# Kernel optimization log

Hardware: AMD Instinct MI355X
Metric: run time of the kernel (lower is better)

## Reference

```python
import jax, jax.numpy as jnp
import numpy as np

N_NODES = 20000
N_EDGES = 200000
N_GRAPHS = 500
F = 512      # num_features
H = 512      # hidden_dim
C = 10       # num_classes
K = 30       # sort-pool k


def setup_inputs() -> dict:
    key = jax.random.key(0)
    ks = jax.random.split(key, 12)
    p = lambda k, shp: (jax.random.normal(k, shp, jnp.float32) * 0.05)
    x = jax.random.normal(ks[0], (N_NODES, F), jnp.float32)
    edge_index = jax.random.randint(ks[1], (2, N_EDGES), 0, N_NODES, dtype=jnp.int32)
    batch = jnp.sort(jax.random.randint(ks[2], (N_NODES,), 0, N_GRAPHS, dtype=jnp.int32))
    return dict(
        x=x, edge_index=edge_index, batch=batch,
        W1=p(ks[3], (F, H)), b1=jnp.zeros((H,), jnp.float32),
        W2=p(ks[4], (H, H)), b2=jnp.zeros((H,), jnp.float32),
        W3=p(ks[5], (H, 1)), b3=jnp.zeros((1,), jnp.float32),
        cw1=p(ks[6], (16, 1, 2 * H + 1)), cb1=jnp.zeros((16,), jnp.float32),
        cw2=p(ks[7], (32, 16, 5)), cb2=jnp.zeros((32,), jnp.float32),
        lw1=p(ks[8], (352, H)), lb1=jnp.zeros((H,), jnp.float32),
        lw2=p(ks[9], (H, C)), lb2=jnp.zeros((C,), jnp.float32),
    )


def gcn_conv(x, W, b, src, dst):
    # PyG GCNConv: add self-loops, symmetric deg^-1/2 normalization, then scatter-add.
    n = x.shape[0]
    loop = jnp.arange(n, dtype=src.dtype)
    s = jnp.concatenate([src, loop])
    d = jnp.concatenate([dst, loop])
    deg = jax.ops.segment_sum(jnp.ones_like(d, dtype=x.dtype), d, num_segments=n)
    dinv = jnp.where(deg > 0, jax.lax.rsqrt(deg), 0.0)
    norm = dinv[s] * dinv[d]                       # [E+N]
    h = x @ W                                      # transform first (in < out ok)
    out = jax.ops.segment_sum(h[s] * norm[:, None], d, num_segments=n)
    return out + b


def global_sort_pool(feat, batch, num_graphs, k):
    # Sort nodes within each graph by last feature channel (descending),
    # keep first k per graph, zero-pad short graphs. Returns [G, k*D].
    n, D = feat.shape
    key = feat[:, -1]
    order = jnp.lexsort((-key, batch))             # primary: batch asc, secondary: key desc
    bs = batch[order]
    fs = feat[order]
    counts = jax.ops.segment_sum(jnp.ones_like(batch, dtype=jnp.int32), batch, num_segments=num_graphs)
    starts = jnp.cumsum(counts) - counts
    rank = jnp.arange(n, dtype=jnp.int32) - starts[bs]
    valid = rank < k
    pooled = jnp.zeros((num_graphs, k, D), feat.dtype).at[
        bs, jnp.clip(rank, 0, k - 1)
    ].add(jnp.where(valid[:, None], fs, 0.0))
    return pooled.reshape(num_graphs, k * D)


def reference(x, edge_index, batch, W1, b1, W2, b2, W3, b3,
              cw1, cb1, cw2, cb2, lw1, lb1, lw2, lb2):
    src, dst = edge_index[0], edge_index[1]
    x1 = jax.nn.elu(gcn_conv(x, W1, b1, src, dst))                 # dropout = identity (eval)
    x2 = jax.nn.elu(gcn_conv(x1, W2, b2, src, dst) + x1)
    out = gcn_conv(x2, W3, b3, src, dst)                           # [N, 1]
    feat = jnp.concatenate([x1, x2, out], axis=-1)                 # [N, 2H+1]
    D = feat.shape[-1]
    z = global_sort_pool(feat, batch, N_GRAPHS, K)                 # [G, K*D]
    z = z[:, None, :]                                              # [G, 1, K*D]
    dn = ('NCH', 'OIH', 'NCH')
    z = jax.nn.relu(jax.lax.conv_general_dilated(z, cw1, (D,), 'VALID', dimension_numbers=dn) + cb1[None, :, None])  # [G,16,30]
    z = jax.lax.reduce_window(z, -jnp.inf, jax.lax.max, (1, 1, 2), (1, 1, 2), 'VALID')                               # [G,16,15]
    z = jax.nn.relu(jax.lax.conv_general_dilated(z, cw2, (1,), 'VALID', dimension_numbers=dn) + cb2[None, :, None])  # [G,32,11]
    z = z.reshape(z.shape[0], -1)                                  # [G,352]
    z = jax.nn.relu(z @ lw1 + lb1)
    return z @ lw2 + lb2                                           # [G, C]
```

## Files before the change

### kernel.cpp

```cpp
#include <hip/hip_runtime.h>
#include <hip/hip_bf16.h>

#define NN 20000
#define NEDGE 200000
#define NG 500
#define KTOP 30
#define HDIM 512

typedef __attribute__((ext_vector_type(8))) short s16x8;
typedef __attribute__((ext_vector_type(4))) float f32x4;

__device__ __forceinline__ unsigned short f2bf(float f) {
    unsigned int u = __float_as_uint(f);
    return (unsigned short)((u + 0x7FFFu + ((u >> 16) & 1u)) >> 16);
}
__device__ __forceinline__ float bf2f(unsigned short s) {
    return __uint_as_float(((unsigned int)s) << 16);
}


__global__ void k_init(int* indeg, int* ccur, int* gcnt) {
    int i = blockIdx.x * 256 + threadIdx.x;
    if (i < NN) { indeg[i] = 0; ccur[i] = 0; }
    if (i < NG) gcnt[i] = 0;
}

__global__ void k_count(const int* __restrict__ dst, int* indeg, int ne) {
    int e = blockIdx.x * 256 + threadIdx.x;
    if (e < ne) atomicAdd(&indeg[dst[e]], 1);
}

__global__ void k_gcount(const int* __restrict__ batch, int* gcnt) {
    int i = blockIdx.x * 256 + threadIdx.x;
    if (i < NN) atomicAdd(&gcnt[batch[i]], 1);
}

__global__ void k_dinv(const int* __restrict__ indeg, float* dinv) {
    int i = blockIdx.x * 256 + threadIdx.x;
    if (i < NN) dinv[i] = rsqrtf((float)(indeg[i] + 1));
}

__global__ void k_scan(const int* __restrict__ in, int* __restrict__ out, int n) {
    const int NT = 256;
    __shared__ int sums[NT];
    int t = threadIdx.x;
    int per = (n + NT - 1) / NT;
    int s0 = t * per;
    int local = 0;
    for (int k = 0; k < per; ++k) { int idx = s0 + k; if (idx < n) local += in[idx]; }
    sums[t] = local;
    __syncthreads();
    for (int off = 1; off < NT; off <<= 1) {
        int v = (t >= off) ? sums[t - off] : 0;
        __syncthreads();
        sums[t] += v;
        __syncthreads();
    }
    int run = sums[t] - local;
    for (int k = 0; k < per; ++k) { int idx = s0 + k; if (idx < n) { out[idx] = run; run += in[idx]; } }
    if (t == NT - 1) out[n] = run;
}

__global__ void k_fill(const int* __restrict__ src, const int* __restrict__ dst,
                       const int* __restrict__ cstart, int* ccur, int* csrc, int ne) {
    int e = blockIdx.x * 256 + threadIdx.x;
    if (e < ne) {
        int d = dst[e];
        int pos = cstart[d] + atomicAdd(&ccur[d], 1);
        csrc[pos] = src[e];
    }
}


__global__ __launch_bounds__(256) void k_split(const float* __restrict__ A,
                                               unsigned short* __restrict__ o0,
                                               unsigned short* __restrict__ o1,
                                               unsigned short* __restrict__ o2, int n4) {
    int i = blockIdx.x * 256 + threadIdx.x;
    if (i >= n4) return;
    float4 v = ((const float4*)A)[i];
    float f[4] = {v.x, v.y, v.z, v.w};
    unsigned short h0[4], h1[4], h2[4];
    #pragma unroll
    for (int j = 0; j < 4; ++j) {
        h0[j] = f2bf(f[j]);   float r = f[j] - bf2f(h0[j]);
        h1[j] = f2bf(r);      r -= bf2f(h1[j]);
        h2[j] = f2bf(r);
    }
    ((ushort4*)o0)[i] = make_ushort4(h0[0], h0[1], h0[2], h0[3]);
    ((ushort4*)o1)[i] = make_ushort4(h1[0], h1[1], h1[2], h1[3]);
    ((ushort4*)o2)[i] = make_ushort4(h2[0], h2[1], h2[2], h2[3]);
}

__global__ __launch_bounds__(256) void k_splitW(const float* __restrict__ W,
                                                unsigned short* __restrict__ w0,
                                                unsigned short* __restrict__ w1,
                                                unsigned short* __restrict__ w2) {
    __shared__ float tile[32][33];
    int bk = blockIdx.x * 32, bn = blockIdx.y * 32;
    int tx = threadIdx.x & 31, ty = threadIdx.x >> 5;
    #pragma unroll
    for (int r = 0; r < 4; ++r)
        tile[ty * 4 + r][tx] = W[(size_t)(bk + ty * 4 + r) * 512 + bn + tx];
    __syncthreads();
    #pragma unroll
    for (int r = 0; r < 4; ++r) {
        int n = bn + ty * 4 + r, k = bk + tx;
        float v = tile[tx][ty * 4 + r];
        unsigned short a0 = f2bf(v); float rr = v - bf2f(a0);
        unsigned short a1 = f2bf(rr); rr -= bf2f(a1);
        w0[(size_t)n * 512 + k] = a0;
        w1[(size_t)n * 512 + k] = a1;
        w2[(size_t)n * 512 + k] = f2bf(rr);
    }
}


#define ASTR (NN * HDIM)
#define BSTR (512 * 512)

__global__ __launch_bounds__(256) void k_gemm_mfma(const unsigned short* __restrict__ S,
                                                   const unsigned short* __restrict__ Wt,
                                                   float* __restrict__ C, int M) {
    __shared__ short lds[6][4096];
    const int t = threadIdx.x;
    const int lane = t & 63, wid = t >> 6;
    const int wr = wid >> 1, wc = wid & 1;
    const int bm = blockIdx.x * 128, bn = blockIdx.y * 128;
    const int arow = lane & 15, koff = (lane >> 4) * 8;

    int offA[6], offB[6], ldsA[6], ldsB[6];
    #pragma unroll
    for (int i = 0; i < 6; ++i) {
        int u = i * 4 + wid;
        int c = u >> 3, g = u & 7;
        int row = bm + g * 16 + arow; if (row >= M) row = M - 1;
        offA[i] = c * ASTR + row * HDIM + koff;
        ldsA[i] = c * 4096 + (g * 64 + lane) * 8;
    }
    #pragma unroll
    for (int i = 0; i < 6; ++i) {
        int u = i * 4 + wid;
        int c = u >> 3, g = u & 7;
        int row = bn + g * 16 + arow;
        offB[i] = c * BSTR + row * 512 + koff;
        ldsB[i] = (3 + c) * 4096 + (g * 64 + lane) * 8;
    }

    f32x4 acc[4][4];
    #pragma unroll
    for (int m = 0; m < 4; ++m)
        #pragma unroll
        for (int n = 0; n < 4; ++n) acc[m][n] = (f32x4){0.f, 0.f, 0.f, 0.f};

    s16x8 stA[6], stB[6];
    #pragma unroll
    for (int i = 0; i < 6; ++i) stA[i] = *(const s16x8*)(S + offA[i]);
    #pragma unroll
    for (int i = 0; i < 6; ++i) stB[i] = *(const s16x8*)(Wt + offB[i]);

    short* lp = &lds[0][0];
    #pragma unroll 1
    for (int s = 0; s < 16; ++s) {
        __syncthreads();
        #pragma unroll
        for (int i = 0; i < 6; ++i) *(s16x8*)(lp + ldsA[i]) = stA[i];
        #pragma unroll
        for (int i = 0; i < 6; ++i) *(s16x8*)(lp + ldsB[i]) = stB[i];
        if (s + 1 < 16) {
            int kadv = (s + 1) * 32;
            #pragma unroll
            for (int i = 0; i < 6; ++i) stA[i] = *(const s16x8*)(S + offA[i] + kadv);
            #pragma unroll
            for (int i = 0; i < 6; ++i) stB[i] = *(const s16x8*)(Wt + offB[i] + kadv);
        }
        __syncthreads();
        s16x8 af[3][4], bf[3][4];
        #pragma unroll
        for (int c = 0; c < 3; ++c)
            #pragma unroll
            for (int m = 0; m < 4; ++m)
                af[c][m] = *(const s16x8*)(lp + c * 4096 + ((wr * 4 + m) * 64 + lane) * 8);
        #pragma unroll
        for (int c = 0; c < 3; ++c)
            #pragma unroll
            for (int n = 0; n < 4; ++n)
                bf[c][n] = *(const s16x8*)(lp + (3 + c) * 4096 + ((wc * 4 + n) * 64 + lane) * 8);
        #pragma unroll
        for (int m = 0; m < 4; ++m)
            #pragma unroll
            for (int n = 0; n < 4; ++n) {
                acc[m][n] = __builtin_amdgcn_mfma_f32_16x16x32_bf16(af[0][m], bf[0][n], acc[m][n], 0, 0, 0);
                acc[m][n] = __builtin_amdgcn_mfma_f32_16x16x32_bf16(af[0][m], bf[1][n], acc[m][n], 0, 0, 0);
                acc[m][n] = __builtin_amdgcn_mfma_f32_16x16x32_bf16(af[1][m], bf[0][n], acc[m][n], 0, 0, 0);
                acc[m][n] = __builtin_amdgcn_mfma_f32_16x16x32_bf16(af[0][m], bf[2][n], acc[m][n], 0, 0, 0);
                acc[m][n] = __builtin_amdgcn_mfma_f32_16x16x32_bf16(af[1][m], bf[1][n], acc[m][n], 0, 0, 0);
                acc[m][n] = __builtin_amdgcn_mfma_f32_16x16x32_bf16(af[2][m], bf[0][n], acc[m][n], 0, 0, 0);
            }
    }

    int crow0 = bm + wr * 64 + (lane >> 4) * 4;
    int ccol0 = bn + wc * 64 + (lane & 15);
    #pragma unroll
    for (int m = 0; m < 4; ++m)
        #pragma unroll
        for (int n = 0; n < 4; ++n)
            #pragma unroll
            for (int r = 0; r < 4; ++r) {
                int row = crow0 + m * 16 + r;
                if (row < M) C[(size_t)row * 512 + ccol0 + n * 16] = acc[m][n][r];
            }
}


__global__ __launch_bounds__(256) void k_agg(const float* __restrict__ h, const int* __restrict__ cstart,
                                             const int* __restrict__ csrc, const float* __restrict__ dinv,
                                             const float* __restrict__ bias, const float* __restrict__ res,
                                             float* __restrict__ out) {
    int w = blockIdx.x * 4 + (threadIdx.x >> 6);
    if (w >= NN) return;
    int lane = threadIdx.x & 63;
    float di = dinv[w];
    float acc[8] = {0, 0, 0, 0, 0, 0, 0, 0};
    int e0 = cstart[w], e1 = cstart[w + 1];
    for (int j = e0; j < e1; ++j) {
        int s = csrc[j];
        float wt = dinv[s] * di;
        const float* hr = h + (size_t)s * HDIM + lane * 8;
        float4 v0 = *(const float4*)hr;
        float4 v1 = *(const float4*)(hr + 4);
        acc[0] = fmaf(v0.x, wt, acc[0]); acc[1] = fmaf(v0.y, wt, acc[1]);
        acc[2] = fmaf(v0.z, wt, acc[2]); acc[3] = fmaf(v0.w, wt, acc[3]);
        acc[4] = fmaf(v1.x, wt, acc[4]); acc[5] = fmaf(v1.y, wt, acc[5]);
        acc[6] = fmaf(v1.z, wt, acc[6]); acc[7] = fmaf(v1.w, wt, acc[7]);
    }
    {
        float wt = di * di;
        const float* hr = h + (size_t)w * HDIM + lane * 8;
        float4 v0 = *(const float4*)hr;
        float4 v1 = *(const float4*)(hr + 4);
        acc[0] = fmaf(v0.x, wt, acc[0]); acc[1] = fmaf(v0.y, wt, acc[1]);
        acc[2] = fmaf(v0.z, wt, acc[2]); acc[3] = fmaf(v0.w, wt, acc[3]);
        acc[4] = fmaf(v1.x, wt, acc[4]); acc[5] = fmaf(v1.y, wt, acc[5]);
        acc[6] = fmaf(v1.z, wt, acc[6]); acc[7] = fmaf(v1.w, wt, acc[7]);
    }
    const float* bptr = bias + lane * 8;
    const float* rptr = res ? res + (size_t)w * HDIM + lane * 8 : nullptr;
    float v[8];
    #pragma unroll
    for (int q = 0; q < 8; ++q) {
        float t = acc[q] + bptr[q];
        if (rptr) t += rptr[q];
        v[q] = t > 0.f ? t : (expf(t) - 1.f);
    }
    float* orow = out + (size_t)w * HDIM + lane * 8;
    *(float4*)orow       = make_float4(v[0], v[1], v[2], v[3]);
    *(float4*)(orow + 4) = make_float4(v[4], v[5], v[6], v[7]);
}


__global__ __launch_bounds__(256) void k_gemv3(const float* __restrict__ x2, const float* __restrict__ W3,
                                               float* __restrict__ h3) {
    int w = blockIdx.x * 4 + (threadIdx.x >> 6);
    if (w >= NN) return;
    int lane = threadIdx.x & 63;
    const float* r = x2 + (size_t)w * HDIM + lane * 8;
    const float* wp = W3 + lane * 8;
    float4 a0 = *(const float4*)r, a1 = *(const float4*)(r + 4);
    float4 w0 = *(const float4*)wp, w1 = *(const float4*)(wp + 4);
    float acc = a0.x * w0.x + a0.y * w0.y + a0.z * w0.z + a0.w * w0.w
              + a1.x * w1.x + a1.y * w1.y + a1.z * w1.z + a1.w * w1.w;
    #pragma unroll
    for (int off = 32; off; off >>= 1) acc += __shfl_down(acc, off);
    if (lane == 0) h3[w] = acc;
}

__global__ void k_agg3(const float* __restrict__ h3, const int* __restrict__ cstart,
                       const int* __restrict__ csrc, const float* __restrict__ dinv,
                       const float* __restrict__ b3, float* __restrict__ key) {
    int i = blockIdx.x * 256 + threadIdx.x;
    if (i >= NN) return;
    float di = dinv[i];
    float acc = h3[i] * di * di;
    int e0 = cstart[i], e1 = cstart[i + 1];
    for (int j = e0; j < e1; ++j) {
        int s = csrc[j];
        acc = fmaf(h3[s], dinv[s] * di, acc);
    }
    key[i] = acc + b3[0];
}


#define MAXN 2048
__global__ __launch_bounds__(256) void k_select(const float* __restrict__ key, const int* __restrict__ gstart,
                                                int* __restrict__ sel) {
    int g = blockIdx.x;
    int s = gstart[g], e = gstart[g + 1];
    int cnt = e - s;
    if (cnt > MAXN) cnt = MAXN;
    __shared__ float ks[MAXN];
    __shared__ int sels[KTOP];
    for (int i = threadIdx.x; i < cnt; i += 256) ks[i] = key[s + i];
    if (threadIdx.x < KTOP) sels[threadIdx.x] = -1;
    __syncthreads();
    for (int i = threadIdx.x; i < cnt; i += 256) {
        float ki = ks[i];
        int r = 0;
        for (int j = 0; j < cnt; ++j) {
            float kj = ks[j];
            r += (kj > ki) || (kj == ki && j < i);
        }
        if (r < KTOP) sels[r] = s + i;
    }
    __syncthreads();
    if (threadIdx.x < KTOP) sel[g * KTOP + threadIdx.x] = sels[threadIdx.x];
}


__global__ __launch_bounds__(256) void k_conv1(const float* __restrict__ x1, const float* __restrict__ x2,
                                               const float* __restrict__ key, const int* __restrict__ sel,
                                               const float* __restrict__ cw1, const float* __restrict__ cb1,
                                               float* __restrict__ c1) {
    int gp = blockIdx.x;
    int g = gp / KTOP, p = gp - g * KTOP;
    int t = threadIdx.x;
    int node = sel[gp];
    if (node < 0) {
        if (t < 16) c1[((size_t)g * 16 + t) * KTOP + p] = fmaxf(cb1[t], 0.f);
        return;
    }
    __shared__ float f[1025];
    __shared__ float red[16][17];
    if (t < 128) {
        ((float4*)f)[t] = ((const float4*)(x1 + (size_t)node * HDIM))[t];
    } else {
        ((float4*)(f + 512))[t - 128] = ((const float4*)(x2 + (size_t)node * HDIM))[t - 128];
    }
    if (t == 0) f[1024] = key[node];
    __syncthreads();
    int oc = t >> 4, ch = t & 15;
    const float* wrow = cw1 + (size_t)oc * 1025;
    float pd = 0.f;
    for (int k = ch; k < 1025; k += 16) pd = fmaf(f[k], wrow[k], pd);
    red[oc][ch] = pd;
    __syncthreads();
    if (t < 16) {
        float ssum = cb1[t];
        #pragma unroll
        for (int c = 0; c < 16; ++c) ssum += red[t][c];
        c1[((size_t)g * 16 + t) * KTOP + p] = fmaxf(ssum, 0.f);
    }
}


__global__ __launch_bounds__(512) void k_head(const float* __restrict__ c1, const float* __restrict__ cw2,
                                              const float* __restrict__ cb2, const float* __restrict__ lw1,
                                              const float* __restrict__ lb1, const float* __restrict__ lw2,
                                              const float* __restrict__ lb2, float* __restrict__ outp) {
    int g = blockIdx.x, t = threadIdx.x;
    __shared__ float m[16][15];
    __shared__ float z2s[352];
    __shared__ float z3[512];
    if (t < 240) {
        int ic = t / 15, q = t % 15;
        const float* row = c1 + ((size_t)g * 16 + ic) * KTOP;
        m[ic][q] = fmaxf(row[2 * q], row[2 * q + 1]);
    }
    __syncthreads();
    if (t < 352) {
        int oc = t / 11, tt = t % 11;
        float acc = cb2[oc];
        #pragma unroll
        for (int ic = 0; ic < 16; ++ic)
            #pragma unroll
            for (int j = 0; j < 5; ++j)
                acc = fmaf(m[ic][tt + j], cw2[((size_t)oc * 16 + ic) * 5 + j], acc);
        z2s[t] = fmaxf(acc, 0.f);
    }
    __syncthreads();
    {
        float acc = lb1[t];
        for (int k = 0; k < 352; ++k) acc = fmaf(z2s[k], lw1[(size_t)k * 512 + t], acc);
        z3[t] = fmaxf(acc, 0.f);
    }
    __syncthreads();
    if (t < 160) {
        int oc = t >> 4, l = t & 15;
        float acc = 0.f;
        for (int k = l; k < 512; k += 16) acc = fmaf(z3[k], lw2[(size_t)k * 10 + oc], acc);
        #pragma unroll
        for (int off = 1; off < 16; off <<= 1) acc += __shfl_xor(acc, off);
        if (l == 0) outp[g * 10 + oc] = acc + lb2[oc];
    }
}


extern "C" void kernel_launch(void* const* d_in, const int* in_sizes, int n_in,
                              void* d_out, int out_size, void* d_ws, size_t ws_size,
                              hipStream_t stream) {
    const float* x    = (const float*)d_in[0];
    const int*   ei   = (const int*)d_in[1];
    const int*   batch= (const int*)d_in[2];
    const float* W1   = (const float*)d_in[3];
    const float* b1   = (const float*)d_in[4];
    const float* W2   = (const float*)d_in[5];
    const float* b2   = (const float*)d_in[6];
    const float* W3   = (const float*)d_in[7];
    const float* b3   = (const float*)d_in[8];
    const float* cw1  = (const float*)d_in[9];
    const float* cb1  = (const float*)d_in[10];
    const float* cw2  = (const float*)d_in[11];
    const float* cb2  = (const float*)d_in[12];
    const float* lw1  = (const float*)d_in[13];
    const float* lb1  = (const float*)d_in[14];
    const float* lw2  = (const float*)d_in[15];
    const float* lb2  = (const float*)d_in[16];

    const int NE = in_sizes[1] / 2;
    const int* srcp = ei;
    const int* dstp = ei + NE;

    char* ws = (char*)d_ws;
    size_t o = 0;
    auto al = [&](size_t b) { size_t r = o; o += (b + 255) & ~(size_t)255; return r; };
    int*   indeg  = (int*)(ws + al((size_t)NN * 4));
    int*   ccur   = (int*)(ws + al((size_t)NN * 4));
    int*   cstart = (int*)(ws + al((size_t)(NN + 1) * 4));
    int*   csrc   = (int*)(ws + al((size_t)NE * 4));
    float* dinv   = (float*)(ws + al((size_t)NN * 4));
    float* h      = (float*)(ws + al((size_t)NN * HDIM * 4));
    float* x1     = (float*)(ws + al((size_t)NN * HDIM * 4));
    float* h3     = (float*)(ws + al((size_t)NN * 4));
    float* key    = (float*)(ws + al((size_t)NN * 4));
    int*   gcnt   = (int*)(ws + al((size_t)NG * 4));
    int*   gstart = (int*)(ws + al((size_t)(NG + 1) * 4));
    int*   sel    = (int*)(ws + al((size_t)NG * KTOP * 4));
    float* c1     = (float*)(ws + al((size_t)NG * 16 * KTOP * 4));
    unsigned short* S  = (unsigned short*)(ws + al((size_t)3 * NN * HDIM * 2));
    unsigned short* Wt = (unsigned short*)(ws + al((size_t)3 * 512 * 512 * 2));
    float* x2 = (float*)S;
    (void)ws_size; (void)n_in; (void)out_size;

    int nb_n = (NN + 255) / 256;
    int nb_e = (NE + 255) / 256;

    k_init<<<nb_n, 256, 0, stream>>>(indeg, ccur, gcnt);
    k_count<<<nb_e, 256, 0, stream>>>(dstp, indeg, NE);
    k_gcount<<<nb_n, 256, 0, stream>>>(batch, gcnt);
    k_dinv<<<nb_n, 256, 0, stream>>>(indeg, dinv);
    k_scan<<<1, 256, 0, stream>>>(indeg, cstart, NN);
    k_scan<<<1, 256, 0, stream>>>(gcnt, gstart, NG);
    k_fill<<<nb_e, 256, 0, stream>>>(srcp, dstp, cstart, ccur, csrc, NE);

    const int n4 = NN * HDIM / 4;
    const int nsp = (n4 + 255) / 256;
    dim3 gw(16, 16);
    dim3 gg((NN + 127) / 128, 4);

    k_split<<<nsp, 256, 0, stream>>>(x, S, S + (size_t)NN * HDIM, S + (size_t)2 * NN * HDIM, n4);
    k_splitW<<<gw, 256, 0, stream>>>(W1, Wt, Wt + 512 * 512, Wt + 2 * 512 * 512);
    k_gemm_mfma<<<gg, 256, 0, stream>>>(S, Wt, h, NN);
    k_agg<<<NN / 4, 256, 0, stream>>>(h, cstart, csrc, dinv, b1, nullptr, x1);
    k_split<<<nsp, 256, 0, stream>>>(x1, S, S + (size_t)NN * HDIM, S + (size_t)2 * NN * HDIM, n4);
    k_splitW<<<gw, 256, 0, stream>>>(W2, Wt, Wt + 512 * 512, Wt + 2 * 512 * 512);
    k_gemm_mfma<<<gg, 256, 0, stream>>>(S, Wt, h, NN);
    k_agg<<<NN / 4, 256, 0, stream>>>(h, cstart, csrc, dinv, b2, x1, x2);
    k_gemv3<<<NN / 4, 256, 0, stream>>>(x2, W3, h3);
    k_agg3<<<nb_n, 256, 0, stream>>>(h3, cstart, csrc, dinv, b3, key);
    k_select<<<NG, 256, 0, stream>>>(key, gstart, sel);
    k_conv1<<<NG * KTOP, 256, 0, stream>>>(x1, x2, key, sel, cw1, cb1, c1);
    k_head<<<NG, 512, 0, stream>>>(c1, cw2, cb2, lw1, lb1, lw2, lb2, (float*)d_out);
}
```

Baseline: 684.0 us.

## Fuse bf16 split into aggregation, halve GEMM M-tile, unroll edge loop by two

The first aggregation kernel now writes the three-way bf16 split of its output directly, which removes a separate k_split pass that re-read x1 from memory. The MFMA GEMM tile shrinks from 128 to 64 rows, doubling the block count to improve occupancy and load balance across CUs, at the cost of more B-tile reloads. The aggregation edge loop is unrolled by two with separate accumulators to keep more gather loads in flight. The extra accumulators slightly change summation order and raise register use.

```diff
diff --git a/kernel.cpp b/kernel.cpp
--- a/kernel.cpp
+++ b/kernel.cpp
@@ -122,21 +122,21 @@
 __global__ __launch_bounds__(256) void k_gemm_mfma(const unsigned short* __restrict__ S,
                                                    const unsigned short* __restrict__ Wt,
                                                    float* __restrict__ C, int M) {
-    __shared__ short lds[6][4096];
+    __shared__ short lds[18432];
     const int t = threadIdx.x;
     const int lane = t & 63, wid = t >> 6;
     const int wr = wid >> 1, wc = wid & 1;
-    const int bm = blockIdx.x * 128, bn = blockIdx.y * 128;
+    const int bm = blockIdx.x * 64, bn = blockIdx.y * 128;
     const int arow = lane & 15, koff = (lane >> 4) * 8;
 
-    int offA[6], offB[6], ldsA[6], ldsB[6];
-    #pragma unroll
-    for (int i = 0; i < 6; ++i) {
+    int offA[3], offB[6], ldsA[3], ldsB[6];
+    #pragma unroll
+    for (int i = 0; i < 3; ++i) {
         int u = i * 4 + wid;
-        int c = u >> 3, g = u & 7;
+        int c = u >> 2, g = u & 3;
         int row = bm + g * 16 + arow; if (row >= M) row = M - 1;
         offA[i] = c * ASTR + row * HDIM + koff;
-        ldsA[i] = c * 4096 + (g * 64 + lane) * 8;
+        ldsA[i] = c * 2048 + (g * 64 + lane) * 8;
     }
     #pragma unroll
     for (int i = 0; i < 6; ++i) {
@@ -144,50 +144,50 @@
         int c = u >> 3, g = u & 7;
         int row = bn + g * 16 + arow;
         offB[i] = c * BSTR + row * 512 + koff;
-        ldsB[i] = (3 + c) * 4096 + (g * 64 + lane) * 8;
-    }
-
-    f32x4 acc[4][4];
-    #pragma unroll
-    for (int m = 0; m < 4; ++m)
+        ldsB[i] = 6144 + c * 4096 + (g * 64 + lane) * 8;
+    }
+
+    f32x4 acc[2][4];
+    #pragma unroll
+    for (int m = 0; m < 2; ++m)
         #pragma unroll
         for (int n = 0; n < 4; ++n) acc[m][n] = (f32x4){0.f, 0.f, 0.f, 0.f};
 
-    s16x8 stA[6], stB[6];
-    #pragma unroll
-    for (int i = 0; i < 6; ++i) stA[i] = *(const s16x8*)(S + offA[i]);
+    s16x8 stA[3], stB[6];
+    #pragma unroll
+    for (int i = 0; i < 3; ++i) stA[i] = *(const s16x8*)(S + offA[i]);
     #pragma unroll
     for (int i = 0; i < 6; ++i) stB[i] = *(const s16x8*)(Wt + offB[i]);
 
-    short* lp = &lds[0][0];
+    short* lp = lds;
     #pragma unroll 1
     for (int s = 0; s < 16; ++s) {
         __syncthreads();
         #pragma unroll
-        for (int i = 0; i < 6; ++i) *(s16x8*)(lp + ldsA[i]) = stA[i];
+        for (int i = 0; i < 3; ++i) *(s16x8*)(lp + ldsA[i]) = stA[i];
         #pragma unroll
         for (int i = 0; i < 6; ++i) *(s16x8*)(lp + ldsB[i]) = stB[i];
         if (s + 1 < 16) {
             int kadv = (s + 1) * 32;
             #pragma unroll
-            for (int i = 0; i < 6; ++i) stA[i] = *(const s16x8*)(S + offA[i] + kadv);
+            for (int i = 0; i < 3; ++i) stA[i] = *(const s16x8*)(S + offA[i] + kadv);
             #pragma unroll
             for (int i = 0; i < 6; ++i) stB[i] = *(const s16x8*)(Wt + offB[i] + kadv);
         }
         __syncthreads();
-        s16x8 af[3][4], bf[3][4];
+        s16x8 af[3][2], bf[3][4];
         #pragma unroll
         for (int c = 0; c < 3; ++c)
             #pragma unroll
-            for (int m = 0; m < 4; ++m)
-                af[c][m] = *(const s16x8*)(lp + c * 4096 + ((wr * 4 + m) * 64 + lane) * 8);
+            for (int m = 0; m < 2; ++m)
+                af[c][m] = *(const s16x8*)(lp + c * 2048 + ((wr * 2 + m) * 64 + lane) * 8);
         #pragma unroll
         for (int c = 0; c < 3; ++c)
             #pragma unroll
             for (int n = 0; n < 4; ++n)
-                bf[c][n] = *(const s16x8*)(lp + (3 + c) * 4096 + ((wc * 4 + n) * 64 + lane) * 8);
-        #pragma unroll
-        for (int m = 0; m < 4; ++m)
+                bf[c][n] = *(const s16x8*)(lp + 6144 + c * 4096 + ((wc * 4 + n) * 64 + lane) * 8);
+        #pragma unroll
+        for (int m = 0; m < 2; ++m)
             #pragma unroll
             for (int n = 0; n < 4; ++n) {
                 acc[m][n] = __builtin_amdgcn_mfma_f32_16x16x32_bf16(af[0][m], bf[0][n], acc[m][n], 0, 0, 0);
@@ -199,10 +199,10 @@
             }
     }
 
-    int crow0 = bm + wr * 64 + (lane >> 4) * 4;
+    int crow0 = bm + wr * 32 + (lane >> 4) * 4;
     int ccol0 = bn + wc * 64 + (lane & 15);
     #pragma unroll
-    for (int m = 0; m < 4; ++m)
+    for (int m = 0; m < 2; ++m)
         #pragma unroll
         for (int n = 0; n < 4; ++n)
             #pragma unroll
@@ -216,14 +216,35 @@
 __global__ __launch_bounds__(256) void k_agg(const float* __restrict__ h, const int* __restrict__ cstart,
                                              const int* __restrict__ csrc, const float* __restrict__ dinv,
                                              const float* __restrict__ bias, const float* __restrict__ res,
-                                             float* __restrict__ out) {
+                                             float* __restrict__ out,
+                                             unsigned short* __restrict__ o0,
+                                             unsigned short* __restrict__ o1,
+                                             unsigned short* __restrict__ o2) {
     int w = blockIdx.x * 4 + (threadIdx.x >> 6);
     if (w >= NN) return;
     int lane = threadIdx.x & 63;
     float di = dinv[w];
     float acc[8] = {0, 0, 0, 0, 0, 0, 0, 0};
+    float acc2[8] = {0, 0, 0, 0, 0, 0, 0, 0};
     int e0 = cstart[w], e1 = cstart[w + 1];
-    for (int j = e0; j < e1; ++j) {
+    int j = e0;
+    for (; j + 1 < e1; j += 2) {
+        int s0 = csrc[j], s1 = csrc[j + 1];
+        float wt0 = dinv[s0] * di, wt1 = dinv[s1] * di;
+        const float* hr0 = h + (size_t)s0 * HDIM + lane * 8;
+        const float* hr1 = h + (size_t)s1 * HDIM + lane * 8;
+        float4 a0 = *(const float4*)hr0, a1 = *(const float4*)(hr0 + 4);
+        float4 b0 = *(const float4*)hr1, b1 = *(const float4*)(hr1 + 4);
+        acc[0] = fmaf(a0.x, wt0, acc[0]); acc[1] = fmaf(a0.y, wt0, acc[1]);
+        acc[2] = fmaf(a0.z, wt0, acc[2]); acc[3] = fmaf(a0.w, wt0, acc[3]);
+        acc[4] = fmaf(a1.x, wt0, acc[4]); acc[5] = fmaf(a1.y, wt0, acc[5]);
+        acc[6] = fmaf(a1.z, wt0, acc[6]); acc[7] = fmaf(a1.w, wt0, acc[7]);
+        acc2[0] = fmaf(b0.x, wt1, acc2[0]); acc2[1] = fmaf(b0.y, wt1, acc2[1]);
+        acc2[2] = fmaf(b0.z, wt1, acc2[2]); acc2[3] = fmaf(b0.w, wt1, acc2[3]);
+        acc2[4] = fmaf(b1.x, wt1, acc2[4]); acc2[5] = fmaf(b1.y, wt1, acc2[5]);
+        acc2[6] = fmaf(b1.z, wt1, acc2[6]); acc2[7] = fmaf(b1.w, wt1, acc2[7]);
+    }
+    if (j < e1) {
         int s = csrc[j];
         float wt = dinv[s] * di;
         const float* hr = h + (size_t)s * HDIM + lane * 8;
@@ -249,13 +270,29 @@
     float v[8];
     #pragma unroll
     for (int q = 0; q < 8; ++q) {
-        float t = acc[q] + bptr[q];
-        if (rptr) t += rptr[q];
-        v[q] = t > 0.f ? t : (expf(t) - 1.f);
+        float tt = acc[q] + acc2[q] + bptr[q];
+        if (rptr) tt += rptr[q];
+        v[q] = tt > 0.f ? tt : (expf(tt) - 1.f);
     }
     float* orow = out + (size_t)w * HDIM + lane * 8;
     *(float4*)orow       = make_float4(v[0], v[1], v[2], v[3]);
     *(float4*)(orow + 4) = make_float4(v[4], v[5], v[6], v[7]);
+    if (o0) {
+        unsigned short h0[8], h1[8], h2[8];
+        #pragma unroll
+        for (int q = 0; q < 8; ++q) {
+            h0[q] = f2bf(v[q]);  float r = v[q] - bf2f(h0[q]);
+            h1[q] = f2bf(r);     r -= bf2f(h1[q]);
+            h2[q] = f2bf(r);
+        }
+        size_t base = (size_t)w * HDIM + lane * 8;
+        *(ushort4*)(o0 + base)     = make_ushort4(h0[0], h0[1], h0[2], h0[3]);
+        *(ushort4*)(o0 + base + 4) = make_ushort4(h0[4], h0[5], h0[6], h0[7]);
+        *(ushort4*)(o1 + base)     = make_ushort4(h1[0], h1[1], h1[2], h1[3]);
+        *(ushort4*)(o1 + base + 4) = make_ushort4(h1[4], h1[5], h1[6], h1[7]);
+        *(ushort4*)(o2 + base)     = make_ushort4(h2[0], h2[1], h2[2], h2[3]);
+        *(ushort4*)(o2 + base + 4) = make_ushort4(h2[4], h2[5], h2[6], h2[7]);
+    }
 }
 
 
@@ -455,16 +492,17 @@
     const int n4 = NN * HDIM / 4;
     const int nsp = (n4 + 255) / 256;
     dim3 gw(16, 16);
-    dim3 gg((NN + 127) / 128, 4);
-
-    k_split<<<nsp, 256, 0, stream>>>(x, S, S + (size_t)NN * HDIM, S + (size_t)2 * NN * HDIM, n4);
+    dim3 gg((NN + 63) / 64, 4);
+    unsigned short* S1 = S + (size_t)NN * HDIM;
+    unsigned short* S2 = S + (size_t)2 * NN * HDIM;
+
+    k_split<<<nsp, 256, 0, stream>>>(x, S, S1, S2, n4);
     k_splitW<<<gw, 256, 0, stream>>>(W1, Wt, Wt + 512 * 512, Wt + 2 * 512 * 512);
     k_gemm_mfma<<<gg, 256, 0, stream>>>(S, Wt, h, NN);
-    k_agg<<<NN / 4, 256, 0, stream>>>(h, cstart, csrc, dinv, b1, nullptr, x1);
-    k_split<<<nsp, 256, 0, stream>>>(x1, S, S + (size_t)NN * HDIM, S + (size_t)2 * NN * HDIM, n4);
+    k_agg<<<NN / 4, 256, 0, stream>>>(h, cstart, csrc, dinv, b1, nullptr, x1, S, S1, S2);
     k_splitW<<<gw, 256, 0, stream>>>(W2, Wt, Wt + 512 * 512, Wt + 2 * 512 * 512);
     k_gemm_mfma<<<gg, 256, 0, stream>>>(S, Wt, h, NN);
-    k_agg<<<NN / 4, 256, 0, stream>>>(h, cstart, csrc, dinv, b2, x1, x2);
+    k_agg<<<NN / 4, 256, 0, stream>>>(h, cstart, csrc, dinv, b2, x1, x2, nullptr, nullptr, nullptr);
     k_gemv3<<<NN / 4, 256, 0, stream>>>(x2, W3, h3);
     k_agg3<<<nb_n, 256, 0, stream>>>(h3, cstart, csrc, dinv, b3, key);
     k_select<<<NG, 256, 0, stream>>>(key, gstart, sel);
```

Result: no change. 672.2 us (-1.7%).
